# Kernel optimization log

Measured on AMD Instinct MI355X. Metric: run time of the kernel, lower is better.

## Reference

```python
import jax, jax.numpy as jnp
import numpy as np

DIM = 1024
NH = 16
HD = DIM // NH  # 64
WS = 14         # window size
DFF = 4 * DIM
EPS = 1e-6


def layernorm(x, scale, bias):
    m = jnp.mean(x, axis=-1, keepdims=True)
    v = jnp.var(x, axis=-1, keepdims=True)
    return (x - m) * jax.lax.rsqrt(v + EPS) * scale + bias


def get_rel_pos(q_size, k_size, rel_pos):
    # table size (2*WS-1, HD) matches max_rel_dist, so no resize needed
    coords = (jnp.arange(q_size)[:, None] - jnp.arange(k_size)[None, :] + (k_size - 1)).astype(jnp.int32)
    return rel_pos[coords.reshape(-1)].reshape(q_size, k_size, -1)  # (q,k,HD)


def window_partition(x):
    b, h, w, c = x.shape
    pad_h = (WS - h % WS) % WS
    pad_w = (WS - w % WS) % WS
    # faithful to source: pad_w applied on axis 1, pad_h on axis 2
    x = jnp.pad(x, ((0, 0), (0, pad_w), (0, pad_h), (0, 0)))
    hp, wp = h + pad_h, w + pad_w
    x = x.reshape(b, hp // WS, WS, wp // WS, WS, c)
    windows = x.transpose(0, 1, 3, 2, 4, 5).reshape(-1, WS, WS, c)
    return windows, (hp, wp)


def window_unpartition(windows, pad_hw, hw):
    hp, wp = pad_hw
    h, w = hw
    b = windows.shape[0] // (hp * wp // WS // WS)
    x = windows.reshape(b, hp // WS, wp // WS, WS, WS, -1)
    x = x.transpose(0, 1, 3, 2, 4, 5).reshape(b, hp, wp, -1)
    return x[:, :h, :w, :]


def attention(x, qkv_kernel, qkv_bias, rel_pos_h, rel_pos_w, proj_kernel, proj_bias):
    b, h, w, _ = x.shape
    qkv = x @ qkv_kernel + qkv_bias                                  # (b,h,w,3*DIM)
    qkv = qkv.reshape(b, h * w, 3, NH, HD).transpose(2, 0, 3, 1, 4)
    qkv = qkv.reshape(3, b * NH, h * w, HD)
    q, k, v = qkv[0], qkv[1], qkv[2]
    attn = (q * HD ** -0.5) @ k.transpose(0, 2, 1)                   # (b*NH, hw, hw)
    rh = get_rel_pos(h, h, rel_pos_h)                                # (h,h,HD)
    rw = get_rel_pos(w, w, rel_pos_w)                                # (w,w,HD)
    r_q = q.reshape(-1, h, w, HD)
    rel_h = jnp.einsum('bhwc,hkc->bhwk', r_q, rh)
    rel_w = jnp.einsum('bhwc,wkc->bhwk', r_q, rw)
    attn = (attn.reshape(-1, h, w, h, w) + rel_h[:, :, :, :, None] + rel_w[:, :, :, None, :]).reshape(-1, h * w, h * w)
    attn = jax.nn.softmax(attn, axis=-1)
    out = (attn @ v).reshape(b, NH, h, w, HD).transpose(0, 2, 3, 1, 4).reshape(b, h, w, DIM)
    return out @ proj_kernel + proj_bias


def setup_inputs() -> dict:
    key = jax.random.key(0)
    ks = jax.random.split(key, 8)
    s = 0.02
    B, H, W = 4, 64, 64
    return {
        'x': jax.random.normal(ks[0], (B, H, W, DIM), jnp.float32),
        'norm1_scale': jnp.ones((DIM,), jnp.float32),
        'norm1_bias': jnp.zeros((DIM,), jnp.float32),
        'qkv_kernel': jax.random.normal(ks[1], (DIM, 3 * DIM), jnp.float32) * s,
        'qkv_bias': jnp.zeros((3 * DIM,), jnp.float32),
        'rel_pos_h': jax.random.normal(ks[2], (2 * WS - 1, HD), jnp.float32) * s,
        'rel_pos_w': jax.random.normal(ks[3], (2 * WS - 1, HD), jnp.float32) * s,
        'proj_kernel': jax.random.normal(ks[4], (DIM, DIM), jnp.float32) * s,
        'proj_bias': jnp.zeros((DIM,), jnp.float32),
        'norm2_scale': jnp.ones((DIM,), jnp.float32),
        'norm2_bias': jnp.zeros((DIM,), jnp.float32),
        'fc1_kernel': jax.random.normal(ks[5], (DIM, DFF), jnp.float32) * s,
        'fc1_bias': jnp.zeros((DFF,), jnp.float32),
        'fc2_kernel': jax.random.normal(ks[6], (DFF, DIM), jnp.float32) * s,
        'fc2_bias': jnp.zeros((DIM,), jnp.float32),
    }


def reference(x, norm1_scale, norm1_bias, qkv_kernel, qkv_bias, rel_pos_h, rel_pos_w,
              proj_kernel, proj_bias, norm2_scale, norm2_bias,
              fc1_kernel, fc1_bias, fc2_kernel, fc2_bias):
    shortcut = x
    h, w = x.shape[1], x.shape[2]
    y = layernorm(x, norm1_scale, norm1_bias)
    y, pad_hw = window_partition(y)
    y = attention(y, qkv_kernel, qkv_bias, rel_pos_h, rel_pos_w, proj_kernel, proj_bias)
    y = window_unpartition(y, pad_hw, (h, w))
    x = shortcut + y                           # drop_path=0, no layer scale
    z = layernorm(x, norm2_scale, norm2_bias)
    z = jax.nn.gelu(z @ fc1_kernel + fc1_bias, approximate=False)
    z = z @ fc2_kernel + fc2_bias
    return x + z
```

## Files before the change

kernel.cpp:

```cpp
#include <hip/hip_runtime.h>

typedef __attribute__((ext_vector_type(8))) short bf16x8;
typedef __attribute__((ext_vector_type(4))) float f32x4;

__device__ __forceinline__ float b2f(ushort u) {
    union { unsigned int i; float f; } v; v.i = ((unsigned int)u) << 16; return v.f;
}
__device__ __forceinline__ ushort f2b(float f) {
    union { float f; unsigned int i; } v; v.f = f;
    unsigned int i = v.i;
    return (ushort)((i + 0x7FFFu + ((i >> 16) & 1u)) >> 16);
}
__device__ __forceinline__ void glds16(const ushort* g, ushort* l) {
    __builtin_amdgcn_global_load_lds((const __attribute__((address_space(1))) void*)g,
                                     (__attribute__((address_space(3))) void*)l, 16, 0, 0);
}
__device__ __forceinline__ void BARX() {
    asm volatile("" ::: "memory");
    __builtin_amdgcn_s_barrier();
    asm volatile("" ::: "memory");
}

__global__ __launch_bounds__(256) void ln_kernel(const float* __restrict__ x,
                                                 const float* __restrict__ sc,
                                                 const float* __restrict__ bi,
                                                 ushort* __restrict__ y) {
    __shared__ float red[8];
    long row = blockIdx.x;
    const float* xr = x + row * 1024;
    int t = threadIdx.x;
    float4 u = *(const float4*)(xr + t * 4);
    float s = u.x + u.y + u.z + u.w;
    float q = u.x * u.x + u.y * u.y + u.z * u.z + u.w * u.w;
    for (int off = 32; off > 0; off >>= 1) {
        s += __shfl_xor(s, off);
        q += __shfl_xor(q, off);
    }
    if ((t & 63) == 0) { red[t >> 6] = s; red[4 + (t >> 6)] = q; }
    __syncthreads();
    s = red[0] + red[1] + red[2] + red[3];
    q = red[4] + red[5] + red[6] + red[7];
    float mean = s * (1.0f / 1024.0f);
    float var = q * (1.0f / 1024.0f) - mean * mean;
    float rstd = rsqrtf(fmaxf(var, 0.0f) + 1e-6f);
    int c = t * 4;
    float o0 = (u.x - mean) * rstd * sc[c + 0] + bi[c + 0];
    float o1 = (u.y - mean) * rstd * sc[c + 1] + bi[c + 1];
    float o2 = (u.z - mean) * rstd * sc[c + 2] + bi[c + 2];
    float o3 = (u.w - mean) * rstd * sc[c + 3] + bi[c + 3];
    uint2 o;
    o.x = (unsigned int)f2b(o0) | ((unsigned int)f2b(o1) << 16);
    o.y = (unsigned int)f2b(o2) | ((unsigned int)f2b(o3) << 16);
    *(uint2*)(y + row * 1024 + c) = o;
}

__global__ __launch_bounds__(256) void ln_part_kernel(const float* __restrict__ x,
                                                      const float* __restrict__ sc,
                                                      const float* __restrict__ bi,
                                                      ushort* __restrict__ wy,
                                                      int win_base, int nvalid) {
    __shared__ float red[8];
    int wt = blockIdx.x;
    int lwin = wt / 196, rr = wt % 196;
    int t = threadIdx.x;
    int valid = 0;
    long xrow = 0;
    if (lwin < nvalid) {
        int gwin = win_base + lwin;
        int img = gwin / 25, wrem = gwin % 25;
        int gh = (wrem / 5) * 14 + rr / 14;
        int gw = (wrem % 5) * 14 + rr % 14;
        if (gh < 64 && gw < 64) {
            valid = 1;
            xrow = (long)img * 4096 + gh * 64 + gw;
        }
    }
    uint2 o; o.x = 0u; o.y = 0u;
    if (valid) {
        const float* xr = x + xrow * 1024;
        float4 u = *(const float4*)(xr + t * 4);
        float s = u.x + u.y + u.z + u.w;
        float q = u.x * u.x + u.y * u.y + u.z * u.z + u.w * u.w;
        for (int off = 32; off > 0; off >>= 1) {
            s += __shfl_xor(s, off);
            q += __shfl_xor(q, off);
        }
        if ((t & 63) == 0) { red[t >> 6] = s; red[4 + (t >> 6)] = q; }
        __syncthreads();
        s = red[0] + red[1] + red[2] + red[3];
        q = red[4] + red[5] + red[6] + red[7];
        float mean = s * (1.0f / 1024.0f);
        float var = q * (1.0f / 1024.0f) - mean * mean;
        float rstd = rsqrtf(fmaxf(var, 0.0f) + 1e-6f);
        int c = t * 4;
        float o0 = (u.x - mean) * rstd * sc[c + 0] + bi[c + 0];
        float o1 = (u.y - mean) * rstd * sc[c + 1] + bi[c + 1];
        float o2 = (u.z - mean) * rstd * sc[c + 2] + bi[c + 2];
        float o3 = (u.w - mean) * rstd * sc[c + 3] + bi[c + 3];
        o.x = (unsigned int)f2b(o0) | ((unsigned int)f2b(o1) << 16);
        o.y = (unsigned int)f2b(o2) | ((unsigned int)f2b(o3) << 16);
    }
    *(uint2*)(wy + (long)wt * 1024 + t * 4) = o;
}

__global__ void transpose_w(const float* __restrict__ in, ushort* __restrict__ out,
                            int K, int N) {
    __shared__ float tile[32][33];
    int n0 = blockIdx.x * 32, k0 = blockIdx.y * 32;
    int tx = threadIdx.x, ty = threadIdx.y;
    for (int i = 0; i < 32; i += 8)
        tile[ty + i][tx] = in[(long)(k0 + ty + i) * N + n0 + tx];
    __syncthreads();
    for (int i = 0; i < 32; i += 8)
        out[(long)(n0 + ty + i) * K + k0 + tx] = f2b(tile[tx][ty + i]);
}

template <int FLAGS, typename OT>
__global__ __launch_bounds__(256) void gemm_bt(const ushort* __restrict__ A,
                                               const ushort* __restrict__ Bt,
                                               const float* __restrict__ bias,
                                               const float* __restrict__ resid,
                                               OT* __restrict__ out,
                                               int M, int N, int K) {
    __shared__ __align__(16) ushort As[128 * 32];
    __shared__ __align__(16) ushort Bs[128 * 32];
    const int tid = threadIdx.x;
    const int lane = tid & 63, w = tid >> 6;
    const int wm = (w >> 1) * 64, wn = (w & 1) * 64;
    const int quad = lane >> 4, l16 = lane & 15;
    const int bm = blockIdx.x * 128, bn = blockIdx.y * 128;
    const int r = tid >> 2, kc = (tid & 3) * 8;
    f32x4 acc[4][4];
#pragma unroll
    for (int i = 0; i < 4; i++)
#pragma unroll
        for (int j = 0; j < 4; j++) acc[i][j] = (f32x4){0.f, 0.f, 0.f, 0.f};
    const ushort* Ag = A + (long)(bm + r) * K + kc;
    const ushort* Bg = Bt + (long)(bn + r) * K + kc;
    ushort* AsW = As + w * 512;
    ushort* BsW = Bs + w * 512;
    for (int k0 = 0; k0 < K; k0 += 32) {
        __syncthreads();
        glds16(Ag + k0, AsW);
        glds16(Ag + (long)64 * K + k0, AsW + 2048);
        glds16(Bg + k0, BsW);
        glds16(Bg + (long)64 * K + k0, BsW + 2048);
        __syncthreads();
        bf16x8 afr[4], bfr[4];
#pragma unroll
        for (int t = 0; t < 4; t++) {
            afr[t] = *(const bf16x8*)&As[(wm + t * 16 + l16) * 32 + quad * 8];
            bfr[t] = *(const bf16x8*)&Bs[(wn + t * 16 + l16) * 32 + quad * 8];
        }
#pragma unroll
        for (int tm = 0; tm < 4; tm++)
#pragma unroll
            for (int tn = 0; tn < 4; tn++)
                acc[tm][tn] = __builtin_amdgcn_mfma_f32_16x16x32_bf16(afr[tm], bfr[tn],
                                                                     acc[tm][tn], 0, 0, 0);
    }
#pragma unroll
    for (int tm = 0; tm < 4; tm++) {
#pragma unroll
        for (int j = 0; j < 4; j++) {
            int gm = bm + wm + tm * 16 + quad * 4 + j;
#pragma unroll
            for (int tn = 0; tn < 4; tn++) {
                int gn = bn + wn + tn * 16 + l16;
                float v = acc[tm][tn][j] + bias[gn];
                if (FLAGS & 1) v = 0.5f * v * (1.0f + erff(v * 0.70710678118654752f));
                if (FLAGS & 2) v += resid[(long)gm * N + gn];
                if (sizeof(OT) == 4) out[(long)gm * N + gn] = (OT)v;
                else out[(long)gm * N + gn] = (OT)f2b(v);
            }
        }
    }
}

#define DSR(dst, addr, imm) \
    asm volatile("ds_read_b128 %0, %1 offset:%2" : "=&v"(dst) : "v"(addr), "n"(imm));

#define MF1(m, n, ar, br) \
    acc[m][n] = __builtin_amdgcn_mfma_f32_16x16x32_bf16(ar, br, acc[m][n], 0, 0, 0);
#define MFROW(m, ar) MF1(m, 0, ar, vb0) MF1(m, 1, ar, vb1) MF1(m, 2, ar, vb2) MF1(m, 3, ar, vb3)

#define SEG(bb, ts, STG, VM) do {                                                        \
    bf16x8 vb0, vb1, vb2, vb3, va0, va1, va2, va3;                                       \
    DSR(vb0, b_addr, (bb) * 16384 + 0)                                                   \
    DSR(vb1, b_addr, (bb) * 16384 + 1024)                                                \
    DSR(vb2, b_addr, (bb) * 16384 + 2048)                                                \
    DSR(vb3, b_addr, (bb) * 16384 + 3072)                                                \
    DSR(va0, a_addr, (bb) * 16384 + 0)                                                   \
    DSR(va1, a_addr, (bb) * 16384 + 1024)                                                \
    DSR(va2, a_addr, (bb) * 16384 + 2048)                                                \
    DSR(va3, a_addr, (bb) * 16384 + 3072)                                                \
    if (STG) {                                                                           \
        glds16(Ag + (long)(ts) * 32, &As[((bb) + 3) & 3][sdst]);                         \
        glds16(Ag2 + (long)(ts) * 32, &As[((bb) + 3) & 3][sdst + 4096]);                 \
        __builtin_amdgcn_sched_barrier(0);                                               \
    }                                                                                    \
    BARX();                                                                              \
    asm volatile("s_waitcnt lgkmcnt(0)" ::: "memory");                                   \
    __builtin_amdgcn_sched_barrier(0);                                                   \
    __builtin_amdgcn_s_setprio(1);                                                       \
    MFROW(0, va0) MFROW(1, va1) MFROW(2, va2) MFROW(3, va3)                              \
    __builtin_amdgcn_s_setprio(0);                                                       \
    BARX();                                                                              \
    DSR(va0, a_addr, (bb) * 16384 + 4096)                                                \
    DSR(va1, a_addr, (bb) * 16384 + 5120)                                                \
    DSR(va2, a_addr, (bb) * 16384 + 6144)                                                \
    DSR(va3, a_addr, (bb) * 16384 + 7168)                                                \
    if (STG) {                                                                           \
        glds16(Bg + (long)(ts) * 32, &Bs[((bb) + 3) & 3][sdst]);                         \
        glds16(Bg2 + (long)(ts) * 32, &Bs[((bb) + 3) & 3][sdst + 4096]);                 \
        __builtin_amdgcn_sched_barrier(0);                                               \
    }                                                                                    \
    BARX();                                                                              \
    asm volatile("s_waitcnt lgkmcnt(0)" ::: "memory");                                   \
    __builtin_amdgcn_sched_barrier(0);                                                   \
    __builtin_amdgcn_s_setprio(1);                                                       \
    MFROW(4, va0) MFROW(5, va1) MFROW(6, va2) MFROW(7, va3)                              \
    __builtin_amdgcn_s_setprio(0);                                                       \
    __builtin_amdgcn_sched_barrier(0);                                                   \
    asm volatile("s_waitcnt " VM ::: "memory");                                          \
    BARX();                                                                              \
} while (0)

template <int FLAGS, typename OT>
__global__ __launch_bounds__(512, 2) void gemm256(const ushort* __restrict__ A,
                                                  const ushort* __restrict__ Bt,
                                                  const float* __restrict__ bias,
                                                  const float* __restrict__ resid,
                                                  OT* __restrict__ out,
                                                  int M, int N, int K, int nbn) {
    __shared__ __align__(64) ushort As[4][8192];
    __shared__ __align__(64) ushort Bs[4][8192];
    const int nwg = gridDim.x;
    const int orig = blockIdx.x;
    const int q8 = nwg >> 3, r8 = nwg & 7;
    const int xcd = orig & 7, sub = orig >> 3;
    const int wgid = (xcd < r8 ? xcd * (q8 + 1) : r8 * (q8 + 1) + (xcd - r8) * q8) + sub;
    const int bm = (wgid / nbn) * 256, bn = (wgid % nbn) * 256;

    const int tid = threadIdx.x;
    const int lane = tid & 63, w = tid >> 6;
    const int quad = lane >> 4, l16 = lane & 15;
    const int wm = (w >> 2) * 128, wn = (w & 3) * 64;

    const int r_st = w * 16 + (lane >> 2);
    const int c_st = (((lane & 3) ^ ((lane >> 2) & 3)) << 3);
    const ushort* Ag = A + (long)(bm + r_st) * K + c_st;
    const ushort* Ag2 = Ag + (long)128 * K;
    const ushort* Bg = Bt + (long)(bn + r_st) * K + c_st;
    const ushort* Bg2 = Bg + (long)128 * K;
    const int sdst = w * 512;

    const int a_base = (wm + l16) * 32 + ((quad ^ (l16 & 3)) << 3);
    const int b_base = (wn + l16) * 32 + ((quad ^ (l16 & 3)) << 3);
    const unsigned a_addr =
        (unsigned)(size_t)(__attribute__((address_space(3))) ushort*)&As[0][0] +
        (unsigned)(a_base * 2);
    const unsigned b_addr =
        (unsigned)(size_t)(__attribute__((address_space(3))) ushort*)&Bs[0][0] +
        (unsigned)(b_base * 2);

    f32x4 acc[8][4];
#pragma unroll
    for (int i = 0; i < 8; i++)
#pragma unroll
        for (int j = 0; j < 4; j++) acc[i][j] = (f32x4){0.f, 0.f, 0.f, 0.f};

    glds16(Ag, &As[0][sdst]);       glds16(Ag2, &As[0][sdst + 4096]);
    glds16(Bg, &Bs[0][sdst]);       glds16(Bg2, &Bs[0][sdst + 4096]);
    glds16(Ag + 32, &As[1][sdst]);  glds16(Ag2 + 32, &As[1][sdst + 4096]);
    glds16(Bg + 32, &Bs[1][sdst]);  glds16(Bg2 + 32, &Bs[1][sdst + 4096]);
    glds16(Ag + 64, &As[2][sdst]);  glds16(Ag2 + 64, &As[2][sdst + 4096]);
    glds16(Bg + 64, &Bs[2][sdst]);  glds16(Bg2 + 64, &Bs[2][sdst + 4096]);
    __builtin_amdgcn_sched_barrier(0);
    asm volatile("s_waitcnt vmcnt(8)" ::: "memory");
    BARX();

    const int nt = K >> 5;
    for (int t = 0; t < nt - 4; t += 4) {
        SEG(0, t + 3, 1, "vmcnt(8)");
        SEG(1, t + 4, 1, "vmcnt(8)");
        SEG(2, t + 5, 1, "vmcnt(8)");
        SEG(3, t + 6, 1, "vmcnt(8)");
    }
    SEG(0, nt - 1, 1, "vmcnt(8)");
    SEG(1, 0, 0, "vmcnt(4)");
    SEG(2, 0, 0, "vmcnt(0)");
    SEG(3, 0, 0, "vmcnt(0)");

#pragma unroll
    for (int m = 0; m < 8; m++) {
#pragma unroll
        for (int j = 0; j < 4; j++) {
            const int gm = bm + wm + m * 16 + quad * 4 + j;
            const long ro = (long)gm * N;
#pragma unroll
            for (int n = 0; n < 4; n++) {
                const int gn = bn + wn + n * 16 + l16;
                float v = acc[m][n][j] + bias[gn];
                if (FLAGS & 1) v = 0.5f * v * (1.0f + erff(v * 0.70710678118654752f));
                if (FLAGS & 2) v += resid[ro + gn];
                if (sizeof(OT) == 4) out[ro + gn] = (OT)v;
                else out[ro + gn] = (OT)f2b(v);
            }
        }
    }
}

__global__ __launch_bounds__(256) void attn_kernel(const ushort* __restrict__ qkv,
                                                   ushort* __restrict__ o_out,
                                                   const float* __restrict__ relH,
                                                   const float* __restrict__ relW,
                                                   int win0, long orow0) {
    __shared__ __align__(16) ushort Vt[64 * 200];
    __shared__ __align__(16) ushort Ps[64 * 104];
    __shared__ __align__(16) ushort sc[8 * 448];
    const int head = blockIdx.y;
    const long qbase = (long)blockIdx.x * 196 * 3072 + head * 64;
    const int gwin = win0 + blockIdx.x;
    const int img = gwin / 25, wrem = gwin % 25;
    const int whh = (wrem / 5) * 14, www = (wrem % 5) * 14;
    const int tid = threadIdx.x, lane = tid & 63, w = tid >> 6;
    const int quad = lane >> 4, l16 = lane & 15;

    for (int idx = tid; idx < 196 * 64; idx += 256) {
        int k = idx >> 6, d = idx & 63;
        Vt[d * 200 + k] = qkv[qbase + 2048 + (long)k * 3072 + d];
    }
    __syncthreads();

    bf16x8 bH[2][2], bW[2][2];
#pragma unroll
    for (int nt = 0; nt < 2; nt++) {
        int n = nt * 16 + l16;
#pragma unroll
        for (int kt = 0; kt < 2; kt++) {
            bf16x8 rh = (bf16x8){0, 0, 0, 0, 0, 0, 0, 0};
            bf16x8 rw = (bf16x8){0, 0, 0, 0, 0, 0, 0, 0};
            if (n < 27) {
                const float* ph = relH + n * 64 + kt * 32 + quad * 8;
                const float* pw = relW + n * 64 + kt * 32 + quad * 8;
#pragma unroll
                for (int e = 0; e < 8; e++) {
                    rh[e] = (short)f2b(ph[e]);
                    rw[e] = (short)f2b(pw[e]);
                }
            }
            bH[nt][kt] = rh;
            bW[nt][kt] = rw;
        }
    }

    for (int tr = w; tr < 13; tr += 4) {
        int qrow = tr * 16 + l16;
        if (qrow > 195) qrow = 195;
        bf16x8 qf0 = *(const bf16x8*)(qkv + qbase + (long)qrow * 3072 + quad * 8);
        bf16x8 qf1 = *(const bf16x8*)(qkv + qbase + (long)qrow * 3072 + 32 + quad * 8);

#pragma unroll
        for (int tab = 0; tab < 2; tab++) {
#pragma unroll
            for (int nt = 0; nt < 2; nt++) {
                f32x4 a = (f32x4){0.f, 0.f, 0.f, 0.f};
                a = __builtin_amdgcn_mfma_f32_16x16x32_bf16(qf0, tab ? bW[nt][0] : bH[nt][0],
                                                            a, 0, 0, 0);
                a = __builtin_amdgcn_mfma_f32_16x16x32_bf16(qf1, tab ? bW[nt][1] : bH[nt][1],
                                                            a, 0, 0, 0);
                int col = nt * 16 + l16;
                if (col < 27) {
#pragma unroll
                    for (int j = 0; j < 4; j++)
                        sc[(w * 2 + tab) * 448 + (quad * 4 + j) * 28 + col] = f2b(a[j]);
                }
            }
        }

        f32x4 sf[13];
#pragma unroll
        for (int tc = 0; tc < 13; tc++) {
            int krow = tc * 16 + l16;
            if (krow > 195) krow = 195;
            const ushort* kp = qkv + qbase + 1024 + (long)krow * 3072 + quad * 8;
            bf16x8 kf0 = *(const bf16x8*)kp;
            bf16x8 kf1 = *(const bf16x8*)(kp + 32);
            f32x4 s = (f32x4){0.f, 0.f, 0.f, 0.f};
            s = __builtin_amdgcn_mfma_f32_16x16x32_bf16(qf0, kf0, s, 0, 0, 0);
            s = __builtin_amdgcn_mfma_f32_16x16x32_bf16(qf1, kf1, s, 0, 0, 0);
            sf[tc] = s;
        }
#pragma unroll
        for (int tc = 0; tc < 13; tc++) {
            int c = tc * 16 + l16;
            if (c < 196) {
                int kh = c / 14, kw = c - kh * 14;
#pragma unroll
                for (int j = 0; j < 4; j++) {
                    int rr = tr * 16 + quad * 4 + j;
                    if (rr > 195) rr = 195;
                    float dh = b2f(sc[(w * 2 + 0) * 448 + (quad * 4 + j) * 28 +
                                      (rr / 14 - kh + 13)]);
                    float dw = b2f(sc[(w * 2 + 1) * 448 + (quad * 4 + j) * 28 +
                                      (rr % 14 - kw + 13)]);
                    sf[tc][j] = sf[tc][j] * 0.125f + dh + dw;
                }
            } else {
#pragma unroll
                for (int j = 0; j < 4; j++) sf[tc][j] = -30000.0f;
            }
        }
        f32x4 mx = sf[0];
#pragma unroll
        for (int tc = 1; tc < 13; tc++)
#pragma unroll
            for (int j = 0; j < 4; j++) mx[j] = fmaxf(mx[j], sf[tc][j]);
        for (int off = 1; off < 16; off <<= 1)
#pragma unroll
            for (int j = 0; j < 4; j++) mx[j] = fmaxf(mx[j], __shfl_xor(mx[j], off));
        f32x4 sum = (f32x4){0.f, 0.f, 0.f, 0.f};
#pragma unroll
        for (int tc = 0; tc < 13; tc++)
#pragma unroll
            for (int j = 0; j < 4; j++) {
                float p = __expf(sf[tc][j] - mx[j]);
                sf[tc][j] = p;
                sum[j] += p;
            }
        for (int off = 1; off < 16; off <<= 1)
#pragma unroll
            for (int j = 0; j < 4; j++) sum[j] += __shfl_xor(sum[j], off);
        f32x4 linv;
#pragma unroll
        for (int j = 0; j < 4; j++) linv[j] = 1.0f / sum[j];

        f32x4 oa[4];
#pragma unroll
        for (int tn = 0; tn < 4; tn++) oa[tn] = (f32x4){0.f, 0.f, 0.f, 0.f};
#pragma unroll
        for (int tc = 0; tc < 6; tc++) {
            int c = tc * 16 + l16;
#pragma unroll
            for (int j = 0; j < 4; j++)
                Ps[(w * 16 + quad * 4 + j) * 104 + c] = f2b(sf[tc][j]);
        }
#pragma unroll
        for (int ks = 0; ks < 3; ks++) {
            bf16x8 pf = *(const bf16x8*)&Ps[(w * 16 + l16) * 104 + ks * 32 + quad * 8];
#pragma unroll
            for (int tn = 0; tn < 4; tn++) {
                bf16x8 vf = *(const bf16x8*)&Vt[(tn * 16 + l16) * 200 + ks * 32 + quad * 8];
                oa[tn] = __builtin_amdgcn_mfma_f32_16x16x32_bf16(pf, vf, oa[tn], 0, 0, 0);
            }
        }
#pragma unroll
        for (int tc = 6; tc < 13; tc++) {
            int c = tc * 16 + l16;
            if (c < 196) {
#pragma unroll
                for (int j = 0; j < 4; j++)
                    Ps[(w * 16 + quad * 4 + j) * 104 + (c - 96)] = f2b(sf[tc][j]);
            }
        }
#pragma unroll
        for (int ks = 0; ks < 3; ks++) {
            bf16x8 pf = *(const bf16x8*)&Ps[(w * 16 + l16) * 104 + ks * 32 + quad * 8];
#pragma unroll
            for (int tn = 0; tn < 4; tn++) {
                bf16x8 vf = *(const bf16x8*)&Vt[(tn * 16 + l16) * 200 + 96 + ks * 32 + quad * 8];
                oa[tn] = __builtin_amdgcn_mfma_f32_16x16x32_bf16(pf, vf, oa[tn], 0, 0, 0);
            }
        }
        for (int kk = 192; kk < 196; kk++) {
            float pj[4];
#pragma unroll
            for (int j = 0; j < 4; j++)
                pj[j] = b2f(Ps[(w * 16 + quad * 4 + j) * 104 + 96 + (kk - 192)]);
#pragma unroll
            for (int tn = 0; tn < 4; tn++) {
                float vv = b2f(Vt[(tn * 16 + l16) * 200 + kk]);
#pragma unroll
                for (int j = 0; j < 4; j++) oa[tn][j] += pj[j] * vv;
            }
        }
#pragma unroll
        for (int j = 0; j < 4; j++) {
            int rr = tr * 16 + quad * 4 + j;
            if (rr < 196) {
                int gh = whh + rr / 14, gw = www + rr % 14;
                if (gh < 64 && gw < 64) {
                    long orow = (long)img * 4096 + gh * 64 + gw - orow0;
#pragma unroll
                    for (int tn = 0; tn < 4; tn++)
                        o_out[orow * 1024 + head * 64 + tn * 16 + l16] =
                            f2b(oa[tn][j] * linv[j]);
                }
            }
        }
    }
}

extern "C" void kernel_launch(void* const* d_in, const int* in_sizes, int n_in,
                              void* d_out, int out_size, void* d_ws, size_t ws_size,
                              hipStream_t stream) {
    const float* x = (const float*)d_in[0];
    const float* n1s = (const float*)d_in[1];
    const float* n1b = (const float*)d_in[2];
    const float* qkvW = (const float*)d_in[3];
    const float* qkvB = (const float*)d_in[4];
    const float* relH = (const float*)d_in[5];
    const float* relW = (const float*)d_in[6];
    const float* projW = (const float*)d_in[7];
    const float* projB = (const float*)d_in[8];
    const float* n2s = (const float*)d_in[9];
    const float* n2b = (const float*)d_in[10];
    const float* fc1W = (const float*)d_in[11];
    const float* fc1B = (const float*)d_in[12];
    const float* fc2W = (const float*)d_in[13];
    const float* fc2B = (const float*)d_in[14];
    float* OUT = (float*)d_out;
    char* ws = (char*)d_ws;

    if (ws_size >= 221000000ULL) {
        ushort* T0  = (ushort*)(ws);
        ushort* TP  = (ushort*)(ws + 6291456ULL);
        ushort* TF1 = (ushort*)(ws + 8388608ULL);
        ushort* TF2 = (ushort*)(ws + 16777216ULL);
        ushort* W0  = (ushort*)(ws + 25165824ULL);
        ushort* QKV = (ushort*)(ws + 65536000ULL);
        ushort* AO  = (ushort*)(ws + 186646528ULL);
        ushort* Z   = (ushort*)(ws + 25165824ULL);
        ushort* H   = (ushort*)(ws + 58720256ULL);

        transpose_w<<<dim3(96, 32), dim3(32, 8), 0, stream>>>(qkvW, T0, 1024, 3072);
        transpose_w<<<dim3(32, 32), dim3(32, 8), 0, stream>>>(projW, TP, 1024, 1024);
        transpose_w<<<dim3(128, 32), dim3(32, 8), 0, stream>>>(fc1W, TF1, 1024, 4096);
        transpose_w<<<dim3(32, 128), dim3(32, 8), 0, stream>>>(fc2W, TF2, 4096, 1024);
        ln_part_kernel<<<19712, 256, 0, stream>>>(x, n1s, n1b, W0, 0, 100);
        gemm256<0, ushort><<<924, 512, 0, stream>>>(W0, T0, qkvB, nullptr, QKV,
                                                    19712, 3072, 1024, 12);
        attn_kernel<<<dim3(100, 16), 256, 0, stream>>>(QKV, AO, relH, relW, 0, 0L);
        gemm256<2, float><<<256, 512, 0, stream>>>(AO, TP, projB, x, OUT,
                                                   16384, 1024, 1024, 4);
        ln_kernel<<<16384, 256, 0, stream>>>(OUT, n2s, n2b, Z);
        gemm256<1, ushort><<<1024, 512, 0, stream>>>(Z, TF1, fc1B, nullptr, H,
                                                     16384, 4096, 1024, 16);
        gemm256<2, float><<<256, 512, 0, stream>>>(H, TF2, fc2B, OUT, OUT,
                                                   16384, 1024, 4096, 4);
    } else if (ws_size >= 100000000ULL) {
        ushort* T0  = (ushort*)(ws);
        ushort* TP  = (ushort*)(ws + 6291456ULL);
        ushort* TF1 = (ushort*)(ws + 8388608ULL);
        ushort* TF2 = (ushort*)(ws + 16777216ULL);
        ushort* AO  = (ushort*)(ws + 25165824ULL);
        ushort* W0  = (ushort*)(ws + 58720256ULL);
        ushort* QKV = (ushort*)(ws + 68943872ULL);
        ushort* Z   = (ushort*)(ws + 25165824ULL);
        ushort* H   = (ushort*)(ws + 58720256ULL);

        transpose_w<<<dim3(96, 32), dim3(32, 8), 0, stream>>>(qkvW, T0, 1024, 3072);
        transpose_w<<<dim3(32, 32), dim3(32, 8), 0, stream>>>(projW, TP, 1024, 1024);
        transpose_w<<<dim3(128, 32), dim3(32, 8), 0, stream>>>(fc1W, TF1, 1024, 4096);
        transpose_w<<<dim3(32, 128), dim3(32, 8), 0, stream>>>(fc2W, TF2, 4096, 1024);
        for (int i = 0; i < 4; i++) {
            ln_part_kernel<<<4992, 256, 0, stream>>>(x, n1s, n1b, W0, i * 25, 25);
            gemm_bt<0, ushort><<<dim3(39, 24), 256, 0, stream>>>(W0, T0, qkvB, nullptr,
                                                                 QKV, 4992, 3072, 1024);
            attn_kernel<<<dim3(25, 16), 256, 0, stream>>>(QKV, AO, relH, relW, i * 25, 0L);
        }
        gemm_bt<2, float><<<dim3(128, 8), 256, 0, stream>>>(AO, TP, projB, x, OUT,
                                                            16384, 1024, 1024);
        for (int c = 0; c < 4; c++) {
            float* xc = OUT + (long)c * 4194304;
            ln_kernel<<<4096, 256, 0, stream>>>(xc, n2s, n2b, Z);
            gemm_bt<1, ushort><<<dim3(32, 32), 256, 0, stream>>>(Z, TF1, fc1B, nullptr, H,
                                                                 4096, 4096, 1024);
            gemm_bt<2, float><<<dim3(32, 8), 256, 0, stream>>>(H, TF2, fc2B, xc, xc,
                                                               4096, 1024, 4096);
        }
    } else {
        ushort* T0 = (ushort*)(ws);
        ushort* W0 = (ushort*)(ws + 6291456ULL);
        ushort* W1 = (ushort*)(ws + 16515072ULL);
        ushort* W2 = (ushort*)(ws + 22806528ULL);
        ushort* F1 = (ushort*)(ws);
        ushort* F2 = (ushort*)(ws + 8388608ULL);
        ushort* Z  = (ushort*)(ws + 16777216ULL);
        ushort* H  = (ushort*)(ws + 18874368ULL);

        transpose_w<<<dim3(96, 32), dim3(32, 8), 0, stream>>>(qkvW, T0, 1024, 3072);
        for (int i = 0; i < 4; i++) {
            const float* xi = x + (long)i * 4194304;
            ln_part_kernel<<<4992, 256, 0, stream>>>(x, n1s, n1b, W0, i * 25, 25);
            for (int g = 0; g < 5; g++) {
                gemm_bt<0, ushort><<<dim3(8, 24), 256, 0, stream>>>(
                    W0 + (long)g * 980 * 1024, T0, qkvB, nullptr, W1, 1024, 3072, 1024);
                attn_kernel<<<dim3(5, 16), 256, 0, stream>>>(W1, W2, relH, relW,
                                                             i * 25 + g * 5, (long)i * 4096);
            }
            transpose_w<<<dim3(32, 32), dim3(32, 8), 0, stream>>>(projW, W1, 1024, 1024);
            gemm_bt<2, float><<<dim3(32, 8), 256, 0, stream>>>(
                W2, W1, projB, xi, OUT + (long)i * 4194304, 4096, 1024, 1024);
        }
        transpose_w<<<dim3(128, 32), dim3(32, 8), 0, stream>>>(fc1W, F1, 1024, 4096);
        transpose_w<<<dim3(32, 128), dim3(32, 8), 0, stream>>>(fc2W, F2, 4096, 1024);
        for (int c = 0; c < 16; c++) {
            float* xc = OUT + (long)c * 1048576;
            ln_kernel<<<1024, 256, 0, stream>>>(xc, n2s, n2b, Z);
            gemm_bt<1, ushort><<<dim3(8, 32), 256, 0, stream>>>(Z, F1, fc1B, nullptr, H,
                                                                1024, 4096, 1024);
            gemm_bt<2, float><<<dim3(8, 8), 256, 0, stream>>>(H, F2, fc2B, xc, xc,
                                                              1024, 1024, 4096);
        }
    }
}
```

Baseline: 908.6 us.

## Switch 256x256 GEMM to 32x32x16 MFMA with new LDS swizzle

Replaces the 16x16x32 bf16 MFMA tiles in the 256-tile GEMM with 32x32x16 MFMAs. Each wave now holds a 4x2 grid of 32x32 accumulators, and the LDS swizzle and read addressing are changed to match the new operand layout. It also collapses the per-segment staging into a single phase, removing two intra-segment barriers and using a partial lgkmcnt wait so MFMA overlaps the remaining LDS reads. The aims are fewer LDS reads per FLOP, higher MFMA throughput and less synchronisation, at the risk of layout or swizzle mistakes and a different epilogue store pattern.

```diff
diff --git a/kernel.cpp b/kernel.cpp
--- a/kernel.cpp
+++ b/kernel.cpp
@@ -2,6 +2,7 @@
 
 typedef __attribute__((ext_vector_type(8))) short bf16x8;
 typedef __attribute__((ext_vector_type(4))) float f32x4;
+typedef __attribute__((ext_vector_type(16))) float f32x16;
 
 __device__ __forceinline__ float b2f(ushort u) {
     union { unsigned int i; float f; } v; v.i = ((unsigned int)u) << 16; return v.f;
@@ -180,46 +181,45 @@
 #define DSR(dst, addr, imm) \
     asm volatile("ds_read_b128 %0, %1 offset:%2" : "=&v"(dst) : "v"(addr), "n"(imm));
 
-#define MF1(m, n, ar, br) \
-    acc[m][n] = __builtin_amdgcn_mfma_f32_16x16x32_bf16(ar, br, acc[m][n], 0, 0, 0);
-#define MFROW(m, ar) MF1(m, 0, ar, vb0) MF1(m, 1, ar, vb1) MF1(m, 2, ar, vb2) MF1(m, 3, ar, vb3)
-
-#define SEG(bb, ts, STG, VM) do {                                                        \
-    bf16x8 vb0, vb1, vb2, vb3, va0, va1, va2, va3;                                       \
-    DSR(vb0, b_addr, (bb) * 16384 + 0)                                                   \
-    DSR(vb1, b_addr, (bb) * 16384 + 1024)                                                \
-    DSR(vb2, b_addr, (bb) * 16384 + 2048)                                                \
-    DSR(vb3, b_addr, (bb) * 16384 + 3072)                                                \
-    DSR(va0, a_addr, (bb) * 16384 + 0)                                                   \
-    DSR(va1, a_addr, (bb) * 16384 + 1024)                                                \
-    DSR(va2, a_addr, (bb) * 16384 + 2048)                                                \
-    DSR(va3, a_addr, (bb) * 16384 + 3072)                                                \
+#define MFMA32(mf, nf, a, b) \
+    acc[mf][nf] = __builtin_amdgcn_mfma_f32_32x32x16_bf16(a, b, acc[mf][nf], 0, 0, 0);
+
+#define TILE32(bb, ts, STG, VM) do {                                                     \
+    bf16x8 b00, b10, a00, a10, a20, a30, b01, b11, a01, a11, a21, a31;                   \
+    DSR(b00, b_k0, (bb) * 16384 + 0)                                                     \
+    DSR(b10, b_k0, (bb) * 16384 + 2048)                                                  \
+    DSR(a00, a_k0, (bb) * 16384 + 0)                                                     \
+    DSR(a10, a_k0, (bb) * 16384 + 2048)                                                  \
+    DSR(a20, a_k0, (bb) * 16384 + 4096)                                                  \
+    DSR(a30, a_k0, (bb) * 16384 + 6144)                                                  \
+    DSR(b01, b_k1, (bb) * 16384 + 0)                                                     \
+    DSR(b11, b_k1, (bb) * 16384 + 2048)                                                  \
+    DSR(a01, a_k1, (bb) * 16384 + 0)                                                     \
+    DSR(a11, a_k1, (bb) * 16384 + 2048)                                                  \
+    DSR(a21, a_k1, (bb) * 16384 + 4096)                                                  \
+    DSR(a31, a_k1, (bb) * 16384 + 6144)                                                  \
     if (STG) {                                                                           \
         glds16(Ag + (long)(ts) * 32, &As[((bb) + 3) & 3][sdst]);                         \
         glds16(Ag2 + (long)(ts) * 32, &As[((bb) + 3) & 3][sdst + 4096]);                 \
-        __builtin_amdgcn_sched_barrier(0);                                               \
+        glds16(Bg + (long)(ts) * 32, &Bs[((bb) + 3) & 3][sdst]);                         \
+        glds16(Bg2 + (long)(ts) * 32, &Bs[((bb) + 3) & 3][sdst + 4096]);                 \
     }                                                                                    \
-    BARX();                                                                              \
+    __builtin_amdgcn_sched_barrier(0);                                                   \
+    asm volatile("s_waitcnt lgkmcnt(6)" ::: "memory");                                   \
+    __builtin_amdgcn_sched_barrier(0);                                                   \
+    __builtin_amdgcn_s_setprio(1);                                                       \
+    MFMA32(0, 0, a00, b00) MFMA32(0, 1, a00, b10)                                        \
+    MFMA32(1, 0, a10, b00) MFMA32(1, 1, a10, b10)                                        \
+    MFMA32(2, 0, a20, b00) MFMA32(2, 1, a20, b10)                                        \
+    MFMA32(3, 0, a30, b00) MFMA32(3, 1, a30, b10)                                        \
+    __builtin_amdgcn_s_setprio(0);                                                       \
     asm volatile("s_waitcnt lgkmcnt(0)" ::: "memory");                                   \
     __builtin_amdgcn_sched_barrier(0);                                                   \
     __builtin_amdgcn_s_setprio(1);                                                       \
-    MFROW(0, va0) MFROW(1, va1) MFROW(2, va2) MFROW(3, va3)                              \
-    __builtin_amdgcn_s_setprio(0);                                                       \
-    BARX();                                                                              \
-    DSR(va0, a_addr, (bb) * 16384 + 4096)                                                \
-    DSR(va1, a_addr, (bb) * 16384 + 5120)                                                \
-    DSR(va2, a_addr, (bb) * 16384 + 6144)                                                \
-    DSR(va3, a_addr, (bb) * 16384 + 7168)                                                \
-    if (STG) {                                                                           \
-        glds16(Bg + (long)(ts) * 32, &Bs[((bb) + 3) & 3][sdst]);                         \
-        glds16(Bg2 + (long)(ts) * 32, &Bs[((bb) + 3) & 3][sdst + 4096]);                 \
-        __builtin_amdgcn_sched_barrier(0);                                               \
-    }                                                                                    \
-    BARX();                                                                              \
-    asm volatile("s_waitcnt lgkmcnt(0)" ::: "memory");                                   \
-    __builtin_amdgcn_sched_barrier(0);                                                   \
-    __builtin_amdgcn_s_setprio(1);                                                       \
-    MFROW(4, va0) MFROW(5, va1) MFROW(6, va2) MFROW(7, va3)                              \
+    MFMA32(0, 0, a01, b01) MFMA32(0, 1, a01, b11)                                        \
+    MFMA32(1, 0, a11, b01) MFMA32(1, 1, a11, b11)                                        \
+    MFMA32(2, 0, a21, b01) MFMA32(2, 1, a21, b11)                                        \
+    MFMA32(3, 0, a31, b01) MFMA32(3, 1, a31, b11)                                        \
     __builtin_amdgcn_s_setprio(0);                                                       \
     __builtin_amdgcn_sched_barrier(0);                                                   \
     asm volatile("s_waitcnt " VM ::: "memory");                                          \
@@ -244,31 +244,37 @@
 
     const int tid = threadIdx.x;
     const int lane = tid & 63, w = tid >> 6;
-    const int quad = lane >> 4, l16 = lane & 15;
+    const int l31 = lane & 31, hi = lane >> 5;
     const int wm = (w >> 2) * 128, wn = (w & 3) * 64;
 
     const int r_st = w * 16 + (lane >> 2);
-    const int c_st = (((lane & 3) ^ ((lane >> 2) & 3)) << 3);
+    const int c_st = (((lane & 3) ^ ((lane >> 2) & 3) ^ ((lane >> 4) & 1)) << 3);
     const ushort* Ag = A + (long)(bm + r_st) * K + c_st;
     const ushort* Ag2 = Ag + (long)128 * K;
     const ushort* Bg = Bt + (long)(bn + r_st) * K + c_st;
     const ushort* Bg2 = Bg + (long)128 * K;
     const int sdst = w * 512;
 
-    const int a_base = (wm + l16) * 32 + ((quad ^ (l16 & 3)) << 3);
-    const int b_base = (wn + l16) * 32 + ((quad ^ (l16 & 3)) << 3);
-    const unsigned a_addr =
-        (unsigned)(size_t)(__attribute__((address_space(3))) ushort*)&As[0][0] +
-        (unsigned)(a_base * 2);
-    const unsigned b_addr =
-        (unsigned)(size_t)(__attribute__((address_space(3))) ushort*)&Bs[0][0] +
-        (unsigned)(b_base * 2);
-
-    f32x4 acc[8][4];
-#pragma unroll
-    for (int i = 0; i < 8; i++)
-#pragma unroll
-        for (int j = 0; j < 4; j++) acc[i][j] = (f32x4){0.f, 0.f, 0.f, 0.f};
+    const int swz = (lane & 3) ^ ((lane >> 2) & 1);
+    const int s0 = swz & 1, s1 = swz >> 1;
+    const int slot_k0 = (((0 ^ s1) << 1) | (hi ^ s0)) << 4;
+    const int slot_k1 = (((1 ^ s1) << 1) | (hi ^ s0)) << 4;
+    const unsigned As0 =
+        (unsigned)(size_t)(__attribute__((address_space(3))) ushort*)&As[0][0];
+    const unsigned Bs0 =
+        (unsigned)(size_t)(__attribute__((address_space(3))) ushort*)&Bs[0][0];
+    const unsigned a_k0 = As0 + (unsigned)((wm + l31) * 64 + slot_k0);
+    const unsigned a_k1 = As0 + (unsigned)((wm + l31) * 64 + slot_k1);
+    const unsigned b_k0 = Bs0 + (unsigned)((wn + l31) * 64 + slot_k0);
+    const unsigned b_k1 = Bs0 + (unsigned)((wn + l31) * 64 + slot_k1);
+
+    f32x16 acc[4][2];
+#pragma unroll
+    for (int i = 0; i < 4; i++)
+#pragma unroll
+        for (int j = 0; j < 2; j++)
+#pragma unroll
+            for (int e = 0; e < 16; e++) acc[i][j][e] = 0.f;
 
     glds16(Ag, &As[0][sdst]);       glds16(Ag2, &As[0][sdst + 4096]);
     glds16(Bg, &Bs[0][sdst]);       glds16(Bg2, &Bs[0][sdst + 4096]);
@@ -282,30 +288,33 @@
 
     const int nt = K >> 5;
     for (int t = 0; t < nt - 4; t += 4) {
-        SEG(0, t + 3, 1, "vmcnt(8)");
-        SEG(1, t + 4, 1, "vmcnt(8)");
-        SEG(2, t + 5, 1, "vmcnt(8)");
-        SEG(3, t + 6, 1, "vmcnt(8)");
-    }
-    SEG(0, nt - 1, 1, "vmcnt(8)");
-    SEG(1, 0, 0, "vmcnt(4)");
-    SEG(2, 0, 0, "vmcnt(0)");
-    SEG(3, 0, 0, "vmcnt(0)");
-
-#pragma unroll
-    for (int m = 0; m < 8; m++) {
-#pragma unroll
-        for (int j = 0; j < 4; j++) {
-            const int gm = bm + wm + m * 16 + quad * 4 + j;
-            const long ro = (long)gm * N;
-#pragma unroll
-            for (int n = 0; n < 4; n++) {
-                const int gn = bn + wn + n * 16 + l16;
-                float v = acc[m][n][j] + bias[gn];
-                if (FLAGS & 1) v = 0.5f * v * (1.0f + erff(v * 0.70710678118654752f));
-                if (FLAGS & 2) v += resid[ro + gn];
-                if (sizeof(OT) == 4) out[ro + gn] = (OT)v;
-                else out[ro + gn] = (OT)f2b(v);
+        TILE32(0, t + 3, 1, "vmcnt(8)");
+        TILE32(1, t + 4, 1, "vmcnt(8)");
+        TILE32(2, t + 5, 1, "vmcnt(8)");
+        TILE32(3, t + 6, 1, "vmcnt(8)");
+    }
+    TILE32(0, nt - 1, 1, "vmcnt(8)");
+    TILE32(1, 0, 0, "vmcnt(4)");
+    TILE32(2, 0, 0, "vmcnt(0)");
+    TILE32(3, 0, 0, "vmcnt(0)");
+
+#pragma unroll
+    for (int mf = 0; mf < 4; mf++) {
+#pragma unroll
+        for (int nf = 0; nf < 2; nf++) {
+            const int gn = bn + wn + nf * 32 + l31;
+#pragma unroll
+            for (int q = 0; q < 4; q++) {
+#pragma unroll
+                for (int j = 0; j < 4; j++) {
+                    const int gm = bm + wm + mf * 32 + q * 8 + j + 4 * hi;
+                    const long ro = (long)gm * N;
+                    float v = acc[mf][nf][q * 4 + j] + bias[gn];
+                    if (FLAGS & 1) v = 0.5f * v * (1.0f + erff(v * 0.70710678118654752f));
+                    if (FLAGS & 2) v += resid[ro + gn];
+                    if (sizeof(OT) == 4) out[ro + gn] = (OT)v;
+                    else out[ro + gn] = (OT)f2b(v);
+                }
             }
         }
     }
```

Result: no change. 901.8 us (-0.7%).
